# Kernel tuning notes

Hardware: AMD Instinct MI355X
Metric: run time of the kernel (lower is better)

## Reference

```python
import jax, jax.numpy as jnp
import numpy as np

D_MODEL = 1024
N_HEADS = 16
HEAD_DIM = D_MODEL // N_HEADS


def setup_inputs() -> dict:
    key = jax.random.key(0)
    ks = jax.random.split(key, 9)
    B, L = 2, 2048
    s = 1.0 / np.sqrt(D_MODEL)
    return {
        "x": jax.random.normal(ks[0], (B, L, D_MODEL), dtype=jnp.float32),
        "q_w": jax.random.normal(ks[1], (D_MODEL, D_MODEL), dtype=jnp.float32) * s,
        "q_b": jnp.zeros((D_MODEL,), dtype=jnp.float32),
        "k_w": jax.random.normal(ks[2], (D_MODEL, D_MODEL), dtype=jnp.float32) * s,
        "k_b": jnp.zeros((D_MODEL,), dtype=jnp.float32),
        "v_w": jax.random.normal(ks[3], (D_MODEL, D_MODEL), dtype=jnp.float32) * s,
        "v_b": jnp.zeros((D_MODEL,), dtype=jnp.float32),
        "o_w": jax.random.normal(ks[4], (D_MODEL, D_MODEL), dtype=jnp.float32) * s,
        "o_b": jnp.zeros((D_MODEL,), dtype=jnp.float32),
    }


def _rope_tables(L, dtype):
    # inv_freq: [head_dim//2]
    inv_freq = 1.0 / (10000.0 ** (jnp.arange(0, HEAD_DIM, 2, dtype=dtype) / HEAD_DIM))
    t = jnp.arange(L, dtype=dtype)
    freqs = t[:, None] * inv_freq[None, :]          # [L, hd/2]
    emb = jnp.concatenate([freqs, freqs], axis=-1)  # [L, hd]
    return jnp.cos(emb), jnp.sin(emb)


def _rotate_half(x):
    x1, x2 = x[..., : HEAD_DIM // 2], x[..., HEAD_DIM // 2 :]
    return jnp.concatenate([-x2, x1], axis=-1)


def reference(x, q_w, q_b, k_w, k_b, v_w, v_b, o_w, o_b):
    B, L, D = x.shape
    H, hd = N_HEADS, HEAD_DIM
    # Linear (torch: x @ W.T + b), then split heads -> [B, H, L, hd]
    def proj(w, b):
        y = jnp.einsum("bld,ed->ble", x, w) + b
        return y.reshape(B, L, H, hd).transpose(0, 2, 1, 3)

    q, k, v = proj(q_w, q_b), proj(k_w, k_b), proj(v_w, v_b)

    cos, sin = _rope_tables(L, x.dtype)  # [L, hd] each, broadcast over B,H
    q = q * cos + _rotate_half(q) * sin
    k = k * cos + _rotate_half(k) * sin

    scores = jnp.einsum("bhqd,bhkd->bhqk", q, k) / jnp.sqrt(jnp.asarray(hd, x.dtype))
    attn = jax.nn.softmax(scores, axis=-1)
    out = jnp.einsum("bhqk,bhkd->bhqd", attn, v)
    out = out.transpose(0, 2, 1, 3).reshape(B, L, D)
    return jnp.einsum("bld,ed->ble", out, o_w) + o_b
```

## Files before the change

### kernel.cpp

```cpp
#include <hip/hip_runtime.h>
#include <math.h>

#define SEQ   2048
#define NH    16
#define HD    64
#define DM    1024
#define BATCH 2
#define MROWS (BATCH*SEQ)

typedef __attribute__((ext_vector_type(8))) short short8;
typedef __attribute__((ext_vector_type(4))) float f32x4;
typedef __attribute__((ext_vector_type(16))) float f32x16;
typedef unsigned short ushort;
typedef unsigned int uint;

__device__ __forceinline__ ushort f2bf(float x){
  unsigned int u = __float_as_uint(x);
  unsigned int r = (u + 0x7fffu + ((u>>16)&1u)) >> 16;
  return (ushort)r;
}
__device__ __forceinline__ float bf2f(ushort h){
  return __uint_as_float(((unsigned int)h) << 16);
}
__device__ __forceinline__ void gload16(const ushort* g, ushort* l){
  __builtin_amdgcn_global_load_lds(
      (const __attribute__((address_space(1))) unsigned int*)(g),
      (__attribute__((address_space(3))) unsigned int*)(l), 16, 0, 0);
}

__global__ void rope_tables_kernel(float* __restrict__ cosT, float* __restrict__ sinT){
  int idx = blockIdx.x*blockDim.x + threadIdx.x;
  if (idx >= SEQ*32) return;
  int i = idx & 31, l = idx >> 5;
  float e = (float)(2*i) / 64.0f;
  float inv = 1.0f / powf(10000.0f, e);
  float ang = (float)l * inv;
  cosT[idx] = cosf(ang);
  sinT[idx] = sinf(ang);
}

__global__ void cast_all_kernel(
    const float* __restrict__ X,
    const float* __restrict__ wq, const float* __restrict__ wk,
    const float* __restrict__ wv, const float* __restrict__ wo,
    ushort* __restrict__ Xh,
    ushort* __restrict__ hq, ushort* __restrict__ hk,
    ushort* __restrict__ hv, ushort* __restrict__ ho)
{
  int idx = blockIdx.x*blockDim.x + threadIdx.x;
  const float* src; ushort* dh; int off;
  const int NX = (MROWS*DM) >> 2;
  if (idx < NX){ src = X; dh = Xh; off = idx; }
  else {
    int t = idx - NX;
    int sel = t >> 18;
    off = t & 262143;
    src = sel==0 ? wq : sel==1 ? wk : sel==2 ? wv : wo;
    dh  = sel==0 ? hq : sel==1 ? hk : sel==2 ? hv : ho;
  }
  float4 v = ((const float4*)src)[off];
  uint2 hp;
  hp.x = (unsigned)f2bf(v.x) | ((unsigned)f2bf(v.y)<<16);
  hp.y = (unsigned)f2bf(v.z) | ((unsigned)f2bf(v.w)<<16);
  ((uint2*)dh)[off] = hp;
}

__global__ __launch_bounds__(256) void gemm_qkv_mfma(
    const ushort* __restrict__ Xh,
    const ushort* __restrict__ Whq, const ushort* __restrict__ Whk, const ushort* __restrict__ Whv,
    const float* __restrict__ bq, const float* __restrict__ bk, const float* __restrict__ bv,
    const float* __restrict__ cosT, const float* __restrict__ sinT,
    ushort* __restrict__ Qb, ushort* __restrict__ Kb, ushort* __restrict__ Vb)
{
  __shared__ __align__(16) ushort Ls[2][128*64];
  ushort* As = Ls[0];
  ushort* Bs = Ls[1];
  const int tid = threadIdx.x, w = tid>>6, lane = tid&63;
  const int c = lane & 15, g = lane >> 4;
  const int wr = w >> 1, wc = w & 1;
  const int m0   = blockIdx.x * 128;
  const int ncat = blockIdx.y * 128;
  const int which = ncat >> 10;
  const int n0    = ncat & 1023;
  const ushort* Bhi = which==0 ? Whq : which==1 ? Whk : Whv;
  const float*  bias= which==0 ? bq  : which==1 ? bk  : bv;

  const int srow = lane >> 3;
  const int scol = ((lane & 7) ^ srow) << 3;

  f32x4 acc[4][4] = {};
  for (int k0 = 0; k0 < DM; k0 += 64){
    __syncthreads();
    #pragma unroll
    for (int i=0;i<4;i++){
      const int rb = w*32 + i*8;
      gload16(Xh  + (size_t)(m0 + rb + srow)*DM + k0 + scol, &As[rb*64]);
      gload16(Bhi + (size_t)(n0 + rb + srow)*DM + k0 + scol, &Bs[rb*64]);
    }
    __syncthreads();
    #pragma unroll
    for (int kc=0;kc<2;kc++){
      short8 a[4], b[4];
      #pragma unroll
      for (int m=0;m<4;m++){
        int row = wr*64 + m*16 + c;
        a[m] = *(const short8*)&As[row*64 + ((((kc<<2)+g) ^ (row&7))<<3)];
      }
      #pragma unroll
      for (int n=0;n<4;n++){
        int row = wc*64 + n*16 + c;
        b[n] = *(const short8*)&Bs[row*64 + ((((kc<<2)+g) ^ (row&7))<<3)];
      }
      #pragma unroll
      for (int m=0;m<4;m++)
        #pragma unroll
        for (int n=0;n<4;n++)
          acc[m][n] = __builtin_amdgcn_mfma_f32_16x16x32_bf16(a[m], b[n], acc[m][n], 0,0,0);
    }
  }

  const int hh = (n0 + wc*64) >> 6;
  if (which == 0){
    #pragma unroll
    for (int m=0;m<4;m++){
      #pragma unroll
      for (int r=0;r<4;r++){
        int mrow = m0 + wr*64 + m*16 + 4*g + r;
        int bb = mrow >> 11, l = mrow & (SEQ-1);
        size_t obase = (((size_t)bb*NH + hh)*SEQ + l)*HD;
        #pragma unroll
        for (int n=0;n<2;n++){
          int d1 = n*16 + c, d2 = d1 + 32;
          float v1 = acc[m][n  ][r] + bias[hh*64 + d1];
          float v2 = acc[m][n+2][r] + bias[hh*64 + d2];
          float co = cosT[l*32 + d1], si = sinT[l*32 + d1];
          Qb[obase + d1] = f2bf((v1*co - v2*si)*0.125f);
          Qb[obase + d2] = f2bf((v2*co + v1*si)*0.125f);
        }
      }
    }
  } else {
    __syncthreads();
    ushort* L0 = Ls[0];
    const int base = (wc*2 + wr)*4096;
    #pragma unroll
    for (int m=0;m<4;m++){
      const int kbl = (m>>1)&1;
      #pragma unroll
      for (int r=0;r<4;r++){
        const int l31 = (m&1)*16 + 4*g + r;
        int mrow = m0 + wr*64 + m*16 + 4*g + r;
        int l = mrow & (SEQ-1);
        #pragma unroll
        for (int n=0;n<2;n++){
          int d1 = n*16 + c, d2 = d1 + 32;
          float v1 = acc[m][n  ][r] + bias[hh*64 + d1];
          float v2 = acc[m][n+2][r] + bias[hh*64 + d2];
          if (which == 1){
            float co = cosT[l*32 + d1], si = sinT[l*32 + d1];
            float o1 = v1*co - v2*si;
            float o2 = v2*co + v1*si;
            L0[base + (kbl*4 + n    )*512 + (l31 + 32*(c>>3))*8 + (c&7)] = f2bf(o1);
            L0[base + (kbl*4 + n + 2)*512 + (l31 + 32*(c>>3))*8 + (c&7)] = f2bf(o2);
          } else {
            int pos = ((n*16 + c) + 32*(g>>1))*8 + 4*(g&1) + r;
            L0[base + (    kbl*2 + (m&1))*512 + pos] = f2bf(v1);
            L0[base + (4 + kbl*2 + (m&1))*512 + pos] = f2bf(v2);
          }
        }
      }
    }
    __syncthreads();
    ushort* Out = (which==1) ? Kb : Vb;
    const int head2 = (n0 + (w>>1)*64) >> 6;
    const int ltile = ((m0 & (SEQ-1)) >> 6) + (w & 1);
    const int bb    = m0 >> 11;
    ushort* dst = Out + (((size_t)bb*NH + head2)*(SEQ/64) + ltile)*4096;
    const ushort* srcl = L0 + w*4096;
    #pragma unroll
    for (int i=0;i<8;i++)
      *(short8*)(dst + i*512 + lane*8) = *(const short8*)(srcl + i*512 + lane*8);
  }
}

__global__ __launch_bounds__(512) void flash_mfma_kernel(
    const ushort* __restrict__ Qb, const ushort* __restrict__ Kb,
    const ushort* __restrict__ Vb, ushort* __restrict__ Opart, float* __restrict__ Ssum)
{
  __shared__ __align__(16) ushort Ks[2][8][512];
  __shared__ __align__(16) ushort Vs[2][8][512];

  const int tid  = threadIdx.x;
  const int w    = tid >> 6;
  const int lane = tid & 63;
  const int c    = lane & 31;
  const int h    = lane >> 5;

  const int hw = blockIdx.x;
  const int lg = (hw & 7)*64 + (hw >> 3);
  const int bx = lg & 7, hd = (lg >> 3) & 15, b = (lg >> 7) & 1, half = lg >> 8;
  const int bh = b*NH + hd;
  const int q0 = bx*256 + w*32;
  const int t0base = half*(SEQ/2);

  const ushort* Kimg = Kb + (size_t)bh*SEQ*HD;
  const ushort* Vimg = Vb + (size_t)bh*SEQ*HD;

  const ushort* Qrow = Qb + ((size_t)bh*SEQ + q0 + c)*HD + 8*h;
  short8 qf[4];
  #pragma unroll
  for (int kc=0;kc<4;kc++) qf[kc] = *(const short8*)(Qrow + kc*16);

  short8 ones;
  #pragma unroll
  for (int i=0;i<8;i++) ones[i] = (short)0x3F80;

  f32x16 oacc[2] = {};
  f32x16 sacc = {};

  #define STAGE(bf, t0) { \
    gload16(Kimg + ((t0)>>6)*4096 + w*512 + lane*8, &Ks[bf][w][0]); \
    gload16(Vimg + ((t0)>>6)*4096 + w*512 + lane*8, &Vs[bf][w][0]); }

  STAGE(0, t0base)
  __syncthreads();

  int buf = 0;
  for (int t = 0; t < SEQ/2; t += 64){
    const int t0 = t0base + t;
    if (t + 64 < SEQ/2){
      STAGE(buf ^ 1, t0 + 64)
    }

    #pragma unroll
    for (int kb=0; kb<2; kb++){
      f32x16 s = {};
      __builtin_amdgcn_s_setprio(1);
      #pragma unroll
      for (int kc=0;kc<4;kc++){
        short8 kf = *(const short8*)&Ks[buf][kb*4+kc][lane*8];
        s = __builtin_amdgcn_mfma_f32_32x32x16_bf16(kf, qf[kc], s, 0,0,0);
      }
      __builtin_amdgcn_s_setprio(0);

      uint pk[8];
      #pragma unroll
      for (int i=0;i<8;i++){
        float p0 = __expf(s[2*i]);
        float p1 = __expf(s[2*i+1]);
        asm("v_cvt_pk_bf16_f32 %0, %1, %2" : "=v"(pk[i]) : "v"(p0), "v"(p1));
      }
      asm volatile("v_permlane32_swap_b32 %0, %1" : "+v"(pk[0]), "+v"(pk[2]));
      asm volatile("v_permlane32_swap_b32 %0, %1" : "+v"(pk[1]), "+v"(pk[3]));
      asm volatile("v_permlane32_swap_b32 %0, %1" : "+v"(pk[4]), "+v"(pk[6]));
      asm volatile("v_permlane32_swap_b32 %0, %1" : "+v"(pk[5]), "+v"(pk[7]));
      short8 pa0, pa1;
      ((uint*)&pa0)[0]=pk[0]; ((uint*)&pa0)[1]=pk[1]; ((uint*)&pa0)[2]=pk[2]; ((uint*)&pa0)[3]=pk[3];
      ((uint*)&pa1)[0]=pk[4]; ((uint*)&pa1)[1]=pk[5]; ((uint*)&pa1)[2]=pk[6]; ((uint*)&pa1)[3]=pk[7];

      __builtin_amdgcn_s_setprio(1);
      #pragma unroll
      for (int db=0; db<2; db++){
        short8 v0 = *(const short8*)&Vs[buf][db*4 + kb*2 + 0][lane*8];
        short8 v1 = *(const short8*)&Vs[buf][db*4 + kb*2 + 1][lane*8];
        oacc[db] = __builtin_amdgcn_mfma_f32_32x32x16_bf16(pa0, v0, oacc[db], 0,0,0);
        oacc[db] = __builtin_amdgcn_mfma_f32_32x32x16_bf16(pa1, v1, oacc[db], 0,0,0);
      }
      sacc = __builtin_amdgcn_mfma_f32_32x32x16_bf16(pa0, ones, sacc, 0,0,0);
      sacc = __builtin_amdgcn_mfma_f32_32x32x16_bf16(pa1, ones, sacc, 0,0,0);
      __builtin_amdgcn_s_setprio(0);
    }

    __syncthreads();
    buf ^= 1;
  }
  #undef STAGE

  ushort* Op = Opart + (size_t)half*MROWS*DM;
  #pragma unroll
  for (int db=0; db<2; db++){
    #pragma unroll
    for (int r=0;r<16;r++){
      int q = q0 + (r&3) + 8*(r>>2) + 4*h;
      Op[((size_t)b*SEQ + q)*DM + hd*HD + db*32 + c] = f2bf(oacc[db][r]);
    }
  }
  if (c == 0){
    float* Sp = Ssum + (size_t)half*BATCH*NH*SEQ + ((size_t)b*NH + hd)*SEQ;
    #pragma unroll
    for (int r=0;r<16;r++){
      int q = q0 + (r&3) + 8*(r>>2) + 4*h;
      Sp[q] = sacc[r];
    }
  }
}

__global__ void combine_kernel(const ushort* __restrict__ Opart, const float* __restrict__ Ssum,
                               ushort* __restrict__ AOh)
{
  const size_t NE = (size_t)MROWS*DM;
  int i = blockIdx.x*blockDim.x + threadIdx.x;
  size_t e = (size_t)i*8;
  int d = (int)(e & (DM-1));
  int q = (int)((e >> 10) & (SEQ-1));
  int b = (int)(e >> 21);
  int hh = d >> 6;
  size_t sidx = ((size_t)b*NH + hh)*SEQ + q;
  float inv = 1.0f / (Ssum[sidx] + Ssum[(size_t)BATCH*NH*SEQ + sidx]);
  short8 a = *(const short8*)(Opart + e);
  short8 bb = *(const short8*)(Opart + NE + e);
  short8 o;
  #pragma unroll
  for (int j=0;j<8;j++)
    o[j] = (short)f2bf((bf2f((ushort)a[j]) + bf2f((ushort)bb[j]))*inv);
  *(short8*)(AOh + e) = o;
}

__global__ __launch_bounds__(256) void gemm_o_mfma(
    const ushort* __restrict__ AOh, const ushort* __restrict__ Who,
    const float* __restrict__ bo, float* __restrict__ Y)
{
  __shared__ __align__(16) ushort As[128*64];
  __shared__ __align__(16) ushort Bs[128*64];
  const int tid = threadIdx.x, w = tid>>6, lane = tid&63;
  const int c = lane & 15, g = lane >> 4;
  const int wr = w >> 1, wc = w & 1;
  const int m0 = blockIdx.x * 128;
  const int n0 = blockIdx.y * 128;

  const int srow = lane >> 3;
  const int scol = ((lane & 7) ^ srow) << 3;

  f32x4 acc[4][4] = {};
  for (int k0 = 0; k0 < DM; k0 += 64){
    __syncthreads();
    #pragma unroll
    for (int i=0;i<4;i++){
      const int rb = w*32 + i*8;
      gload16(AOh + (size_t)(m0 + rb + srow)*DM + k0 + scol, &As[rb*64]);
      gload16(Who + (size_t)(n0 + rb + srow)*DM + k0 + scol, &Bs[rb*64]);
    }
    __syncthreads();
    #pragma unroll
    for (int kc=0;kc<2;kc++){
      short8 a[4], b[4];
      #pragma unroll
      for (int m=0;m<4;m++){
        int row = wr*64 + m*16 + c;
        a[m] = *(const short8*)&As[row*64 + ((((kc<<2)+g) ^ (row&7))<<3)];
      }
      #pragma unroll
      for (int n=0;n<4;n++){
        int row = wc*64 + n*16 + c;
        b[n] = *(const short8*)&Bs[row*64 + ((((kc<<2)+g) ^ (row&7))<<3)];
      }
      #pragma unroll
      for (int m=0;m<4;m++)
        #pragma unroll
        for (int n=0;n<4;n++)
          acc[m][n] = __builtin_amdgcn_mfma_f32_16x16x32_bf16(a[m], b[n], acc[m][n], 0,0,0);
    }
  }

  #pragma unroll
  for (int m=0;m<4;m++){
    #pragma unroll
    for (int r=0;r<4;r++){
      int mrow = m0 + wr*64 + m*16 + 4*g + r;
      #pragma unroll
      for (int n=0;n<4;n++){
        int ncol = n0 + wc*64 + n*16 + c;
        Y[(size_t)mrow*DM + ncol] = acc[m][n][r] + bo[ncol];
      }
    }
  }
}

extern "C" void kernel_launch(void* const* d_in, const int* in_sizes, int n_in,
                              void* d_out, int out_size, void* d_ws, size_t ws_size,
                              hipStream_t stream)
{
  const float* x  = (const float*)d_in[0];
  const float* qw = (const float*)d_in[1];
  const float* qb = (const float*)d_in[2];
  const float* kw = (const float*)d_in[3];
  const float* kb = (const float*)d_in[4];
  const float* vw = (const float*)d_in[5];
  const float* vb = (const float*)d_in[6];
  const float* ow = (const float*)d_in[7];
  const float* ob = (const float*)d_in[8];
  float* out = (float*)d_out;

  const size_t NE = (size_t)MROWS*DM;
  const size_t WE = (size_t)DM*DM;
  float* cosT = (float*)d_ws;
  float* sinT = cosT + SEQ*32;
  float* Ssum = sinT + SEQ*32;
  ushort* p = (ushort*)(Ssum + 2*BATCH*NH*SEQ);
  ushort* Xh  = p;            p += NE;
  ushort* Whq = p;            p += WE;
  ushort* Whk = p;            p += WE;
  ushort* Whv = p;            p += WE;
  ushort* Who = p;            p += WE;
  ushort* Qb  = p;            p += NE;
  ushort* Kb  = p;            p += NE;
  ushort* Vb  = p;            p += NE;
  ushort* Opart = p;          p += 2*NE;
  ushort* AOh = p;            p += NE;

  hipLaunchKernelGGL(rope_tables_kernel, dim3((SEQ*32+255)/256), dim3(256), 0, stream, cosT, sinT);
  hipLaunchKernelGGL(cast_all_kernel, dim3((NE/4 + WE)/256), dim3(256), 0, stream,
                     x, qw, kw, vw, ow, Xh, Whq, Whk, Whv, Who);
  hipLaunchKernelGGL(gemm_qkv_mfma, dim3(MROWS/128, 3072/128), dim3(256), 0, stream,
                     Xh, Whq, Whk, Whv, qb, kb, vb, cosT, sinT, Qb, Kb, Vb);
  hipLaunchKernelGGL(flash_mfma_kernel, dim3(512), dim3(512), 0, stream,
                     Qb, Kb, Vb, Opart, Ssum);
  hipLaunchKernelGGL(combine_kernel, dim3(MROWS*DM/8/256), dim3(256), 0, stream,
                     Opart, Ssum, AOh);
  hipLaunchKernelGGL(gemm_o_mfma, dim3(MROWS/128, DM/128), dim3(256), 0, stream,
                     AOh, Who, ob, out);
}
```

Baseline: 128.9 us.

## Split K/V tiled-image repacking into separate kernel and compute row sums with VALU

The QKV GEMM now writes K and V in plain row layout, the same path as Q, and drops its LDS-staged epilogue that built the tiled MFMA image. A new imagize kernel reads those rows and rearranges them into the tiled K/V images the flash kernel consumes. Separately, the flash kernel stops computing softmax row sums with two extra MFMAs against a ones vector. It instead accumulates the exp values in a scalar register and combines the two half-waves with a permlane swap. The costs are an extra kernel launch plus a full read and rewrite of K and V. Opart now aliases the Krow/Vrow buffers, which are dead by the time flash runs.

```diff
diff --git a/kernel.cpp b/kernel.cpp
--- a/kernel.cpp
+++ b/kernel.cpp
@@ -70,11 +70,10 @@
     const ushort* __restrict__ Whq, const ushort* __restrict__ Whk, const ushort* __restrict__ Whv,
     const float* __restrict__ bq, const float* __restrict__ bk, const float* __restrict__ bv,
     const float* __restrict__ cosT, const float* __restrict__ sinT,
-    ushort* __restrict__ Qb, ushort* __restrict__ Kb, ushort* __restrict__ Vb)
-{
-  __shared__ __align__(16) ushort Ls[2][128*64];
-  ushort* As = Ls[0];
-  ushort* Bs = Ls[1];
+    ushort* __restrict__ Qb, ushort* __restrict__ Krow, ushort* __restrict__ Vrow)
+{
+  __shared__ __align__(16) ushort As[128*64];
+  __shared__ __align__(16) ushort Bs[128*64];
   const int tid = threadIdx.x, w = tid>>6, lane = tid&63;
   const int c = lane & 15, g = lane >> 4;
   const int wr = w >> 1, wc = w & 1;
@@ -120,67 +119,83 @@
   }
 
   const int hh = (n0 + wc*64) >> 6;
-  if (which == 0){
-    #pragma unroll
-    for (int m=0;m<4;m++){
-      #pragma unroll
-      for (int r=0;r<4;r++){
-        int mrow = m0 + wr*64 + m*16 + 4*g + r;
-        int bb = mrow >> 11, l = mrow & (SEQ-1);
-        size_t obase = (((size_t)bb*NH + hh)*SEQ + l)*HD;
-        #pragma unroll
-        for (int n=0;n<2;n++){
-          int d1 = n*16 + c, d2 = d1 + 32;
-          float v1 = acc[m][n  ][r] + bias[hh*64 + d1];
-          float v2 = acc[m][n+2][r] + bias[hh*64 + d2];
+  ushort* Out = which==0 ? Qb : which==1 ? Krow : Vrow;
+  #pragma unroll
+  for (int m=0;m<4;m++){
+    #pragma unroll
+    for (int r=0;r<4;r++){
+      int mrow = m0 + wr*64 + m*16 + 4*g + r;
+      int bb = mrow >> 11, l = mrow & (SEQ-1);
+      size_t obase = (((size_t)bb*NH + hh)*SEQ + l)*HD;
+      #pragma unroll
+      for (int n=0;n<2;n++){
+        int d1 = n*16 + c, d2 = d1 + 32;
+        float v1 = acc[m][n  ][r] + bias[hh*64 + d1];
+        float v2 = acc[m][n+2][r] + bias[hh*64 + d2];
+        if (which < 2){
           float co = cosT[l*32 + d1], si = sinT[l*32 + d1];
-          Qb[obase + d1] = f2bf((v1*co - v2*si)*0.125f);
-          Qb[obase + d2] = f2bf((v2*co + v1*si)*0.125f);
+          float o1 = v1*co - v2*si;
+          float o2 = v2*co + v1*si;
+          if (which == 0){ o1 *= 0.125f; o2 *= 0.125f; }
+          Out[obase + d1] = f2bf(o1);
+          Out[obase + d2] = f2bf(o2);
+        } else {
+          Out[obase + d1] = f2bf(v1);
+          Out[obase + d2] = f2bf(v2);
         }
       }
     }
-  } else {
-    __syncthreads();
-    ushort* L0 = Ls[0];
-    const int base = (wc*2 + wr)*4096;
-    #pragma unroll
-    for (int m=0;m<4;m++){
-      const int kbl = (m>>1)&1;
-      #pragma unroll
-      for (int r=0;r<4;r++){
-        const int l31 = (m&1)*16 + 4*g + r;
-        int mrow = m0 + wr*64 + m*16 + 4*g + r;
-        int l = mrow & (SEQ-1);
-        #pragma unroll
-        for (int n=0;n<2;n++){
-          int d1 = n*16 + c, d2 = d1 + 32;
-          float v1 = acc[m][n  ][r] + bias[hh*64 + d1];
-          float v2 = acc[m][n+2][r] + bias[hh*64 + d2];
-          if (which == 1){
-            float co = cosT[l*32 + d1], si = sinT[l*32 + d1];
-            float o1 = v1*co - v2*si;
-            float o2 = v2*co + v1*si;
-            L0[base + (kbl*4 + n    )*512 + (l31 + 32*(c>>3))*8 + (c&7)] = f2bf(o1);
-            L0[base + (kbl*4 + n + 2)*512 + (l31 + 32*(c>>3))*8 + (c&7)] = f2bf(o2);
-          } else {
-            int pos = ((n*16 + c) + 32*(g>>1))*8 + 4*(g&1) + r;
-            L0[base + (    kbl*2 + (m&1))*512 + pos] = f2bf(v1);
-            L0[base + (4 + kbl*2 + (m&1))*512 + pos] = f2bf(v2);
-          }
-        }
-      }
-    }
-    __syncthreads();
-    ushort* Out = (which==1) ? Kb : Vb;
-    const int head2 = (n0 + (w>>1)*64) >> 6;
-    const int ltile = ((m0 & (SEQ-1)) >> 6) + (w & 1);
-    const int bb    = m0 >> 11;
-    ushort* dst = Out + (((size_t)bb*NH + head2)*(SEQ/64) + ltile)*4096;
-    const ushort* srcl = L0 + w*4096;
-    #pragma unroll
-    for (int i=0;i<8;i++)
-      *(short8*)(dst + i*512 + lane*8) = *(const short8*)(srcl + i*512 + lane*8);
-  }
+  }
+}
+
+__global__ __launch_bounds__(256) void imagize_kernel(
+    const ushort* __restrict__ Krow, const ushort* __restrict__ Vrow,
+    ushort* __restrict__ Kimg, ushort* __restrict__ Vimg)
+{
+  __shared__ __align__(16) ushort Lk[4096];
+  __shared__ __align__(16) ushort Lv[4096];
+  const int tid  = threadIdx.x;
+  const int tile = blockIdx.x & 31;
+  const int bh   = blockIdx.x >> 5;
+  const size_t rbase = ((size_t)bh*SEQ + tile*64)*HD;
+
+  const int l  = tid >> 2;
+  const int d0 = (tid & 3) * 16;
+  const int l31 = l & 31;
+  const int kbl = (l >> 5) & 1;
+
+  short8 a0 = *(const short8*)(Krow + rbase + (size_t)l*HD + d0);
+  short8 a1 = *(const short8*)(Krow + rbase + (size_t)l*HD + d0 + 8);
+  short8 v0 = *(const short8*)(Vrow + rbase + (size_t)l*HD + d0);
+  short8 v1 = *(const short8*)(Vrow + rbase + (size_t)l*HD + d0 + 8);
+
+  {
+    int ch = kbl*4 + (d0>>4);
+    *(short8*)&Lk[ch*512 + l31*8]      = a0;
+    *(short8*)&Lk[ch*512 + (l31+32)*8] = a1;
+  }
+  {
+    const int chb  = kbl*2 + ((l>>4)&1);
+    const int posl = 32*((l>>3)&1);
+    const int l7   = l & 7;
+    #pragma unroll
+    for (int j=0;j<8;j++){
+      int d = d0 + j;
+      Lv[((d>>5)*4 + chb)*512 + ((d&31) + posl)*8 + l7] = (ushort)v0[j];
+    }
+    #pragma unroll
+    for (int j=0;j<8;j++){
+      int d = d0 + 8 + j;
+      Lv[((d>>5)*4 + chb)*512 + ((d&31) + posl)*8 + l7] = (ushort)v1[j];
+    }
+  }
+  __syncthreads();
+
+  const size_t ibase = ((size_t)bh*(SEQ/64) + tile)*4096;
+  *(short8*)(Kimg + ibase + tid*16)     = *(const short8*)&Lk[tid*16];
+  *(short8*)(Kimg + ibase + tid*16 + 8) = *(const short8*)&Lk[tid*16 + 8];
+  *(short8*)(Vimg + ibase + tid*16)     = *(const short8*)&Lv[tid*16];
+  *(short8*)(Vimg + ibase + tid*16 + 8) = *(const short8*)&Lv[tid*16 + 8];
 }
 
 __global__ __launch_bounds__(512) void flash_mfma_kernel(
@@ -211,12 +226,8 @@
   #pragma unroll
   for (int kc=0;kc<4;kc++) qf[kc] = *(const short8*)(Qrow + kc*16);
 
-  short8 ones;
-  #pragma unroll
-  for (int i=0;i<8;i++) ones[i] = (short)0x3F80;
-
   f32x16 oacc[2] = {};
-  f32x16 sacc = {};
+  float ssum = 0.f;
 
   #define STAGE(bf, t0) { \
     gload16(Kimg + ((t0)>>6)*4096 + w*512 + lane*8, &Ks[bf][w][0]); \
@@ -248,6 +259,7 @@
       for (int i=0;i<8;i++){
         float p0 = __expf(s[2*i]);
         float p1 = __expf(s[2*i+1]);
+        ssum += p0 + p1;
         asm("v_cvt_pk_bf16_f32 %0, %1, %2" : "=v"(pk[i]) : "v"(p0), "v"(p1));
       }
       asm volatile("v_permlane32_swap_b32 %0, %1" : "+v"(pk[0]), "+v"(pk[2]));
@@ -266,8 +278,6 @@
         oacc[db] = __builtin_amdgcn_mfma_f32_32x32x16_bf16(pa0, v0, oacc[db], 0,0,0);
         oacc[db] = __builtin_amdgcn_mfma_f32_32x32x16_bf16(pa1, v1, oacc[db], 0,0,0);
       }
-      sacc = __builtin_amdgcn_mfma_f32_32x32x16_bf16(pa0, ones, sacc, 0,0,0);
-      sacc = __builtin_amdgcn_mfma_f32_32x32x16_bf16(pa1, ones, sacc, 0,0,0);
       __builtin_amdgcn_s_setprio(0);
     }
 
@@ -275,6 +285,12 @@
     buf ^= 1;
   }
   #undef STAGE
+
+  {
+    float a = ssum, bsw = ssum;
+    asm volatile("v_permlane32_swap_b32 %0, %1" : "+v"(a), "+v"(bsw));
+    ssum = a + bsw;
+  }
 
   ushort* Op = Opart + (size_t)half*MROWS*DM;
   #pragma unroll
@@ -285,13 +301,9 @@
       Op[((size_t)b*SEQ + q)*DM + hd*HD + db*32 + c] = f2bf(oacc[db][r]);
     }
   }
-  if (c == 0){
+  if (h == 0){
     float* Sp = Ssum + (size_t)half*BATCH*NH*SEQ + ((size_t)b*NH + hd)*SEQ;
-    #pragma unroll
-    for (int r=0;r<16;r++){
-      int q = q0 + (r&3) + 8*(r>>2) + 4*h;
-      Sp[q] = sacc[r];
-    }
+    Sp[q0 + c] = ssum;
   }
 }
 
@@ -397,24 +409,28 @@
   float* sinT = cosT + SEQ*32;
   float* Ssum = sinT + SEQ*32;
   ushort* p = (ushort*)(Ssum + 2*BATCH*NH*SEQ);
-  ushort* Xh  = p;            p += NE;
-  ushort* Whq = p;            p += WE;
-  ushort* Whk = p;            p += WE;
-  ushort* Whv = p;            p += WE;
-  ushort* Who = p;            p += WE;
-  ushort* Qb  = p;            p += NE;
-  ushort* Kb  = p;            p += NE;
-  ushort* Vb  = p;            p += NE;
-  ushort* Opart = p;          p += 2*NE;
-  ushort* AOh = p;            p += NE;
+  ushort* Xh   = p;           p += NE;
+  ushort* Whq  = p;           p += WE;
+  ushort* Whk  = p;           p += WE;
+  ushort* Whv  = p;           p += WE;
+  ushort* Who  = p;           p += WE;
+  ushort* Qb   = p;           p += NE;
+  ushort* Krow = p;           p += NE;
+  ushort* Vrow = p;           p += NE;
+  ushort* Kimg = p;           p += NE;
+  ushort* Vimg = p;           p += NE;
+  ushort* AOh  = p;           p += NE;
+  ushort* Opart = Krow;
 
   hipLaunchKernelGGL(rope_tables_kernel, dim3((SEQ*32+255)/256), dim3(256), 0, stream, cosT, sinT);
   hipLaunchKernelGGL(cast_all_kernel, dim3((NE/4 + WE)/256), dim3(256), 0, stream,
                      x, qw, kw, vw, ow, Xh, Whq, Whk, Whv, Who);
   hipLaunchKernelGGL(gemm_qkv_mfma, dim3(MROWS/128, 3072/128), dim3(256), 0, stream,
-                     Xh, Whq, Whk, Whv, qb, kb, vb, cosT, sinT, Qb, Kb, Vb);
+                     Xh, Whq, Whk, Whv, qb, kb, vb, cosT, sinT, Qb, Krow, Vrow);
+  hipLaunchKernelGGL(imagize_kernel, dim3(BATCH*NH*(SEQ/64)), dim3(256), 0, stream,
+                     Krow, Vrow, Kimg, Vimg);
   hipLaunchKernelGGL(flash_mfma_kernel, dim3(512), dim3(512), 0, stream,
-                     Qb, Kb, Vb, Opart, Ssum);
+                     Qb, Kimg, Vimg, Opart, Ssum);
   hipLaunchKernelGGL(combine_kernel, dim3(MROWS*DM/8/256), dim3(256), 0, stream,
                      Opart, Ssum, AOh);
   hipLaunchKernelGGL(gemm_o_mfma, dim3(MROWS/128, DM/128), dim3(256), 0, stream,
```

New measurement: 129.9 us. No clear change (+0.8%).
